# Kernel tuning notes

Measured on AMD Instinct MI355X. Metric: run time of the kernel, lower is better.

The kernel has to match this reference:

```python
import jax, jax.numpy as jnp
import numpy as np

DIST_SCALE = 10000.0   # divisor in kernel()
KERNEL_EPS = 0.0001    # additive epsilon before reciprocal


def setup_inputs() -> dict:
    key = jax.random.key(0)
    k1, k2, k3 = jax.random.split(key, 3)
    batch, keysize, dict_size, categories = 4096, 512, 16384, 128
    x = jax.random.normal(k1, (batch, keysize), dtype=jnp.float32)
    # keras TruncatedNormal(mean=0, stddev=3) approximated by scaled normal
    keys = 3.0 * jax.random.normal(k2, (dict_size, keysize), dtype=jnp.float32)
    V = jax.random.normal(k3, (dict_size, categories), dtype=jnp.float32)
    return {"x": x, "keys": keys, "V": V}


def reference(x, keys, V):
    # sq_distance(keys, x): (dict_size, batch)
    sq = (
        jnp.sum(keys * keys, axis=1, keepdims=True)            # (D, 1)
        - 2.0 * jnp.einsum("dk,bk->db", keys, x)               # (D, B)
        + jnp.sum(x * x, axis=1)[None, :]                      # (1, B)
    )
    kern = 1.0 / (sq / DIST_SCALE + KERNEL_EPS)                # (D, B)
    KV = jnp.einsum("db,dc->bc", kern, V)                      # (B, C)
    # original: diag(1 / (KV @ ones)) @ KV  ==  row-normalize by row sum
    return KV / jnp.sum(KV, axis=1, keepdims=True)
```

## Files before the change

kernel.cpp:

```cpp
#include <hip/hip_runtime.h>

#define BATCH 4096
#define DICT  16384
#define KDIM  512
#define CAT   128
#define ND    16
#define DSLICE (DICT/ND)
#define DCH   64
#define BT    256

typedef __attribute__((ext_vector_type(4))) float          f32x4;
typedef __attribute__((ext_vector_type(8))) short          short8;
typedef __attribute__((ext_vector_type(8))) unsigned short ushort8;
typedef __attribute__((ext_vector_type(4))) int            intx4;

__device__ __forceinline__ unsigned short f2bf(float f) {
  unsigned int u = __float_as_uint(f);
  return (unsigned short)((u + 0x7fffu + ((u >> 16) & 1u)) >> 16);
}

__device__ __forceinline__ unsigned int cvtpk_bf16(float lo, float hi) {
  unsigned int r;
  asm volatile("v_cvt_pk_bf16_f32 %0, %1, %2" : "=v"(r) : "v"(lo), "v"(hi));
  return r;
}

#define AS1 __attribute__((address_space(1)))
#define AS3 __attribute__((address_space(3)))
__device__ __forceinline__ void gl_lds16(const void* g, void* l) {
  __builtin_amdgcn_global_load_lds((AS1 void*)(g), (AS3 void*)(l), 16, 0, 0);
}

template <int N>
__device__ __forceinline__ void waitv() {
  if constexpr (N == 0)      asm volatile("s_waitcnt vmcnt(0)" ::: "memory");
  else if constexpr (N == 5) asm volatile("s_waitcnt vmcnt(5)" ::: "memory");
  else                       asm volatile("s_waitcnt vmcnt(6)" ::: "memory");
  __builtin_amdgcn_sched_barrier(0);
}

#define MFMA16(a, b, c) __builtin_amdgcn_mfma_f32_16x16x32_bf16((a), (b), (c), 0, 0, 0)

__global__ void prep_rows(const float* __restrict__ in,
                          unsigned short* __restrict__ ob,
                          float* __restrict__ sums) {
  const int lane = threadIdx.x & 63, wv = threadIdx.x >> 6;
  const int row = blockIdx.x * 4 + wv;
  const float* rp = in + ((size_t)row << 9);
  float4 a = *(const float4*)(rp + lane * 8);
  float4 b = *(const float4*)(rp + lane * 8 + 4);
  float s = a.x*a.x + a.y*a.y + a.z*a.z + a.w*a.w
          + b.x*b.x + b.y*b.y + b.z*b.z + b.w*b.w;
  ushort8 o;
  o[0]=f2bf(a.x); o[1]=f2bf(a.y); o[2]=f2bf(a.z); o[3]=f2bf(a.w);
  o[4]=f2bf(b.x); o[5]=f2bf(b.y); o[6]=f2bf(b.z); o[7]=f2bf(b.w);
  *(ushort8*)(ob + ((size_t)row << 9) + lane * 8) = o;
  #pragma unroll
  for (int m = 32; m; m >>= 1) s += __shfl_xor(s, m);
  if (lane == 0) sums[row] = s;
}

__global__ void prep_vt(const float* __restrict__ V,
                        unsigned short* __restrict__ Vt) {
  __shared__ float t[64][129];
  const int d0 = blockIdx.x * 64;
  const int tid = threadIdx.x;
  #pragma unroll
  for (int j = 0; j < 32; ++j) {
    int idx = j * 256 + tid;
    t[idx >> 7][idx & 127] = V[((size_t)d0 << 7) + idx];
  }
  __syncthreads();
  #pragma unroll
  for (int j = 0; j < 32; ++j) {
    int idx = j * 256 + tid;
    int cc = idx >> 6, dd = idx & 63;
    int p = dd & 31, qq = p >> 3, jj = p & 7;
    int src = (dd & 32) + 4 * qq + ((jj < 4) ? jj : (12 + jj));
    Vt[((size_t)cc << 14) + d0 + dd] = f2bf(t[src][cc]);
  }
}

__global__ __launch_bounds__(512, 2)
void varkeys_fused(const unsigned short* __restrict__ xb,
                   const unsigned short* __restrict__ kb,
                   const unsigned short* __restrict__ vt,
                   const float* __restrict__ sx,
                   const float* __restrict__ sk,
                   float* __restrict__ kvp) {
  __shared__ __attribute__((aligned(16))) char lds[131072];
  char* const VsB = lds + 81920;

  const int tid  = threadIdx.x;
  const int lane = tid & 63;
  const int wv   = tid >> 6;
  const int c    = lane & 15;
  const int h    = lane >> 4;
  const int sw   = (lane & 7) << 4;
  const int l3   = lane >> 3;

  const int bid    = blockIdx.x;
  const int btile  = bid & 15;
  const int dslice = bid >> 4;
  const int b0     = btile * BT;
  const int dbase  = dslice * DSLICE;

  const float sxv0 = sx[b0 + wv * 32 + c];
  const float sxv1 = sx[b0 + wv * 32 + 16 + c];

  const int rowA  = wv * 8 + l3;
  const int rowB0 = wv * 32 + l3;
  const int ofs   = (((lane & 7) ^ l3) << 4);

  const char* xbB = (const char*)xb;
  const char* kbB = (const char*)kb;
  const char* vtB = (const char*)vt;

  const f32x4 zero = {0.f, 0.f, 0.f, 0.f};
  f32x4 acc[2][8];
  #pragma unroll
  for (int i = 0; i < 2; ++i)
    #pragma unroll
    for (int j = 0; j < 8; ++j) acc[i][j] = zero;

  gl_lds16(kbB + ((size_t)(dbase + rowA) << 10) + ofs, lds + wv * 1024);
  #pragma unroll
  for (int r = 0; r < 4; ++r)
    gl_lds16(xbB + ((size_t)(b0 + rowB0 + r * 8) << 10) + ofs,
             lds + 16384 + (wv * 4 + r) * 1024);

  f32x4 skq[4];

  for (int dc = 0; dc < DSLICE / DCH; ++dc) {
    const int dg = dbase + dc * DCH;

    f32x4 S[4][2];
    #pragma unroll
    for (int i = 0; i < 4; ++i) { S[i][0] = zero; S[i][1] = zero; }

    #pragma unroll
    for (int kk = 0; kk < 8; ++kk) {
      __builtin_amdgcn_s_barrier();
      if (kk == 0) {
        #pragma unroll
        for (int i = 0; i < 4; ++i)
          skq[i] = *(const f32x4*)(sk + dg + i * 16 + h * 4);
      }
      if (!(kk == 7 && dc == (DSLICE / DCH - 1))) {
        const int dg2 = (kk == 7) ? dg + DCH : dg;
        const int kb2 = ((kk + 1) & 7) << 7;
        char* A2 = lds + ((kk + 1) & 1) * 8192;
        char* B2 = lds + 16384 + ((kk + 1) & 1) * 32768;
        gl_lds16(kbB + ((size_t)(dg2 + rowA) << 10) + kb2 + ofs, A2 + wv * 1024);
        #pragma unroll
        for (int r = 0; r < 4; ++r)
          gl_lds16(xbB + ((size_t)(b0 + rowB0 + r * 8) << 10) + kb2 + ofs,
                   B2 + (wv * 4 + r) * 1024);
        if (kk == 3)
          gl_lds16(vtB + ((size_t)(wv * 8 + l3) << 15) + ((size_t)dg << 1) + ofs,
                   VsB + wv * 1024);
        if (kk == 4)
          gl_lds16(vtB + ((size_t)(64 + wv * 8 + l3) << 15) + ((size_t)dg << 1) + ofs,
                   VsB + 8192 + wv * 1024);
      }
      if (kk == 7) { if (dc == DSLICE / DCH - 1) waitv<0>(); else waitv<5>(); }
      else if (kk == 3 || kk == 4) waitv<6>();
      else waitv<5>();
      __builtin_amdgcn_s_barrier();
      __builtin_amdgcn_sched_barrier(0);

      const char* As = lds + (kk & 1) * 8192;
      const char* Bs = lds + 16384 + (kk & 1) * 32768;
      #pragma unroll
      for (int kf = 0; kf < 2; ++kf) {
        const int ko = (kf * 64 + h * 16) ^ sw;
        short8 bf0 = *(const short8*)(Bs + ((wv * 32 + c) << 7) + ko);
        short8 bf1 = *(const short8*)(Bs + ((wv * 32 + 16 + c) << 7) + ko);
        #pragma unroll
        for (int i = 0; i < 4; ++i) {
          short8 af = *(const short8*)(As + ((i * 16 + c) << 7) + ko);
          S[i][0] = MFMA16(af, bf0, S[i][0]);
          S[i][1] = MFMA16(af, bf1, S[i][1]);
        }
      }
    }

    #pragma unroll
    for (int dk = 0; dk < 2; ++dk) {
      short8 pa[2];
      #pragma unroll
      for (int fj = 0; fj < 2; ++fj) {
        const float sxv = fj ? sxv1 : sxv0;
        const f32x4 sA = S[2 * dk][fj];
        const f32x4 sB = S[2 * dk + 1][fj];
        const f32x4 kA = skq[2 * dk];
        const f32x4 kB = skq[2 * dk + 1];
        float a0 = 10000.f * __builtin_amdgcn_rcpf(kA[0] + sxv - 2.f * sA[0] + 1.f);
        float a1 = 10000.f * __builtin_amdgcn_rcpf(kA[1] + sxv - 2.f * sA[1] + 1.f);
        float a2 = 10000.f * __builtin_amdgcn_rcpf(kA[2] + sxv - 2.f * sA[2] + 1.f);
        float a3 = 10000.f * __builtin_amdgcn_rcpf(kA[3] + sxv - 2.f * sA[3] + 1.f);
        float b0f = 10000.f * __builtin_amdgcn_rcpf(kB[0] + sxv - 2.f * sB[0] + 1.f);
        float b1f = 10000.f * __builtin_amdgcn_rcpf(kB[1] + sxv - 2.f * sB[1] + 1.f);
        float b2f = 10000.f * __builtin_amdgcn_rcpf(kB[2] + sxv - 2.f * sB[2] + 1.f);
        float b3f = 10000.f * __builtin_amdgcn_rcpf(kB[3] + sxv - 2.f * sB[3] + 1.f);
        intx4 fw;
        fw[0] = (int)cvtpk_bf16(a0, a1);
        fw[1] = (int)cvtpk_bf16(a2, a3);
        fw[2] = (int)cvtpk_bf16(b0f, b1f);
        fw[3] = (int)cvtpk_bf16(b2f, b3f);
        pa[fj] = *(short8*)&fw;
      }
      const int ko = (dk * 64 + h * 16) ^ sw;
      #pragma unroll
      for (int fc = 0; fc < 8; ++fc) {
        short8 vb = *(const short8*)(VsB + ((fc * 16 + c) << 7) + ko);
        acc[0][fc] = MFMA16(pa[0], vb, acc[0][fc]);
        acc[1][fc] = MFMA16(pa[1], vb, acc[1][fc]);
      }
    }
  }

  __syncthreads();
  float* eb = (float*)(lds + (wv << 14));
  #pragma unroll
  for (int fb = 0; fb < 2; ++fb)
    #pragma unroll
    for (int r = 0; r < 4; ++r) {
      const int brow = fb * 16 + h * 4 + r;
      #pragma unroll
      for (int fc = 0; fc < 8; ++fc)
        eb[(brow << 7) + fc * 16 + c] = acc[fb][fc][r];
    }
  float* op = kvp + (((size_t)dslice * BATCH + b0 + wv * 32) << 7);
  #pragma unroll
  for (int t = 0; t < 16; ++t) {
    const int row = t * 2 + (lane >> 5);
    f32x4 v = *(const f32x4*)(eb + (row << 7) + ((lane & 31) << 2));
    *(f32x4*)(op + (((size_t)row) << 7) + ((lane & 31) << 2)) = v;
  }
}

__global__ void reduce_norm(const float* __restrict__ part, float* __restrict__ out) {
  const int lane = threadIdx.x & 63, wv = threadIdx.x >> 6;
  const int b = blockIdx.x * 4 + wv;
  float v0 = 0.f, v1 = 0.f;
  #pragma unroll
  for (int s = 0; s < ND; ++s) {
    const float* p = part + ((((size_t)s << 12) + b) << 7);
    v0 += p[lane]; v1 += p[lane + 64];
  }
  float t = v0 + v1;
  #pragma unroll
  for (int m = 32; m; m >>= 1) t += __shfl_xor(t, m);
  out[((size_t)b << 7) + lane]      = v0 / t;
  out[((size_t)b << 7) + lane + 64] = v1 / t;
}

extern "C" void kernel_launch(void* const* d_in, const int* in_sizes, int n_in,
                              void* d_out, int out_size, void* d_ws, size_t ws_size,
                              hipStream_t stream) {
  (void)in_sizes; (void)n_in; (void)out_size; (void)ws_size;
  const float* x    = (const float*)d_in[0];
  const float* keys = (const float*)d_in[1];
  const float* V    = (const float*)d_in[2];
  float* out = (float*)d_out;
  char* ws = (char*)d_ws;
  unsigned short* xb = (unsigned short*)(ws);
  unsigned short* kb = (unsigned short*)(ws + ((size_t)4 << 20));
  unsigned short* vt = (unsigned short*)(ws + ((size_t)20 << 20));
  float* sx  = (float*)(ws + ((size_t)24 << 20));
  float* sk  = (float*)(ws + ((size_t)24 << 20) + (1 << 16));
  float* kvp = (float*)(ws + ((size_t)25 << 20));

  prep_rows<<<BATCH / 4, 256, 0, stream>>>(x, xb, sx);
  prep_rows<<<DICT / 4, 256, 0, stream>>>(keys, kb, sk);
  prep_vt<<<DICT / 64, 256, 0, stream>>>(V, vt);
  varkeys_fused<<<(BATCH / BT) * ND, 512, 0, stream>>>(xb, kb, vt, sx, sk, kvp);
  reduce_norm<<<BATCH / 4, 256, 0, stream>>>(kvp, out);
}
```

Before: 135.1 us.

## Enlarge per-wave tile to 128x64 with 4 waves per block

Each workgroup now uses 256 threads (4 waves) and processes a 128-wide dictionary chunk. Each wave computes a 128x64 distance tile instead of 64x32, and the V tile is split into two halves loaded across k-steps. The goal is more MFMA work per LDS fragment load and fewer barriers per unit of compute, which raises register-level reuse. In exchange, accumulators and S tiles grow to about 256 AGPR/VGPR values per lane, which risks spills and low occupancy (one block per CU). The epilogue now stores the output through LDS cooperatively across the whole block.

After: 157.7 us. 16.7% more time.

```diff
diff --git a/kernel.cpp b/kernel.cpp
--- a/kernel.cpp
+++ b/kernel.cpp
@@ -6,7 +6,7 @@
 #define CAT   128
 #define ND    16
 #define DSLICE (DICT/ND)
-#define DCH   64
+#define DCH   128
 #define BT    256
 
 typedef __attribute__((ext_vector_type(4))) float          f32x4;
@@ -33,9 +33,9 @@
 
 template <int N>
 __device__ __forceinline__ void waitv() {
-  if constexpr (N == 0)      asm volatile("s_waitcnt vmcnt(0)" ::: "memory");
-  else if constexpr (N == 5) asm volatile("s_waitcnt vmcnt(5)" ::: "memory");
-  else                       asm volatile("s_waitcnt vmcnt(6)" ::: "memory");
+  if constexpr (N == 0)       asm volatile("s_waitcnt vmcnt(0)" ::: "memory");
+  else if constexpr (N == 12) asm volatile("s_waitcnt vmcnt(12)" ::: "memory");
+  else                        asm volatile("s_waitcnt vmcnt(14)" ::: "memory");
   __builtin_amdgcn_sched_barrier(0);
 }
 
@@ -81,7 +81,7 @@
   }
 }
 
-__global__ __launch_bounds__(512, 2)
+__global__ __launch_bounds__(256, 1)
 void varkeys_fused(const unsigned short* __restrict__ xb,
                    const unsigned short* __restrict__ kb,
                    const unsigned short* __restrict__ vt,
@@ -89,7 +89,8 @@
                    const float* __restrict__ sk,
                    float* __restrict__ kvp) {
   __shared__ __attribute__((aligned(16))) char lds[131072];
-  char* const VsB = lds + 81920;
+  char* const VsA = lds + 98304;
+  char* const VsB = lds + 114688;
 
   const int tid  = threadIdx.x;
   const int lane = tid & 63;
@@ -105,138 +106,158 @@
   const int b0     = btile * BT;
   const int dbase  = dslice * DSLICE;
 
-  const float sxv0 = sx[b0 + wv * 32 + c];
-  const float sxv1 = sx[b0 + wv * 32 + 16 + c];
-
-  const int rowA  = wv * 8 + l3;
-  const int rowB0 = wv * 32 + l3;
-  const int ofs   = (((lane & 7) ^ l3) << 4);
+  float sxv[4];
+  #pragma unroll
+  for (int fj = 0; fj < 4; ++fj) sxv[fj] = sx[b0 + wv * 64 + fj * 16 + c];
+
+  const int rowS = wv * 8 + l3;
+  const int ofs  = (((lane & 7) ^ l3) << 4);
 
   const char* xbB = (const char*)xb;
   const char* kbB = (const char*)kb;
   const char* vtB = (const char*)vt;
 
   const f32x4 zero = {0.f, 0.f, 0.f, 0.f};
-  f32x4 acc[2][8];
-  #pragma unroll
-  for (int i = 0; i < 2; ++i)
-    #pragma unroll
-    for (int j = 0; j < 8; ++j) acc[i][j] = zero;
-
-  gl_lds16(kbB + ((size_t)(dbase + rowA) << 10) + ofs, lds + wv * 1024);
-  #pragma unroll
-  for (int r = 0; r < 4; ++r)
-    gl_lds16(xbB + ((size_t)(b0 + rowB0 + r * 8) << 10) + ofs,
-             lds + 16384 + (wv * 4 + r) * 1024);
-
-  f32x4 skq[4];
+  f32x4 acc[4][8];
+  #pragma unroll
+  for (int j = 0; j < 4; ++j)
+    #pragma unroll
+    for (int n = 0; n < 8; ++n) acc[j][n] = zero;
+
+  auto stageAB = [&](int ns) {
+    const int dg2 = dbase + (ns >> 3) * DCH;
+    const int kb2 = (ns & 7) << 7;
+    char* A2 = lds + (ns & 1) * 16384;
+    char* B2 = lds + 32768 + (ns & 1) * 32768;
+    #pragma unroll
+    for (int cl = 0; cl < 4; ++cl)
+      gl_lds16(kbB + ((size_t)(dg2 + cl * 32 + rowS) << 10) + kb2 + ofs,
+               A2 + cl * 4096 + wv * 1024);
+    #pragma unroll
+    for (int cl = 0; cl < 8; ++cl)
+      gl_lds16(xbB + ((size_t)(b0 + cl * 32 + rowS) << 10) + kb2 + ofs,
+               B2 + cl * 4096 + wv * 1024);
+  };
+
+  stageAB(0);
+
+  f32x4 skq[8];
 
   for (int dc = 0; dc < DSLICE / DCH; ++dc) {
     const int dg = dbase + dc * DCH;
 
-    f32x4 S[4][2];
-    #pragma unroll
-    for (int i = 0; i < 4; ++i) { S[i][0] = zero; S[i][1] = zero; }
+    f32x4 S[8][4];
+    #pragma unroll
+    for (int i = 0; i < 8; ++i)
+      #pragma unroll
+      for (int fj = 0; fj < 4; ++fj) S[i][fj] = zero;
 
     #pragma unroll
     for (int kk = 0; kk < 8; ++kk) {
       __builtin_amdgcn_s_barrier();
       if (kk == 0) {
         #pragma unroll
-        for (int i = 0; i < 4; ++i)
+        for (int i = 0; i < 8; ++i)
           skq[i] = *(const f32x4*)(sk + dg + i * 16 + h * 4);
       }
-      if (!(kk == 7 && dc == (DSLICE / DCH - 1))) {
-        const int dg2 = (kk == 7) ? dg + DCH : dg;
-        const int kb2 = ((kk + 1) & 7) << 7;
-        char* A2 = lds + ((kk + 1) & 1) * 8192;
-        char* B2 = lds + 16384 + ((kk + 1) & 1) * 32768;
-        gl_lds16(kbB + ((size_t)(dg2 + rowA) << 10) + kb2 + ofs, A2 + wv * 1024);
-        #pragma unroll
-        for (int r = 0; r < 4; ++r)
-          gl_lds16(xbB + ((size_t)(b0 + rowB0 + r * 8) << 10) + kb2 + ofs,
-                   B2 + (wv * 4 + r) * 1024);
-        if (kk == 3)
-          gl_lds16(vtB + ((size_t)(wv * 8 + l3) << 15) + ((size_t)dg << 1) + ofs,
-                   VsB + wv * 1024);
-        if (kk == 4)
-          gl_lds16(vtB + ((size_t)(64 + wv * 8 + l3) << 15) + ((size_t)dg << 1) + ofs,
-                   VsB + 8192 + wv * 1024);
+      const int ns = dc * 8 + kk + 1;
+      if (ns < 64) stageAB(ns);
+      if (kk >= 2 && kk <= 5) {
+        char* const VsH = (kk < 4) ? VsA : VsB;
+        const int hv = (kk < 4) ? 0 : 1;
+        #pragma unroll
+        for (int t = 0; t < 2; ++t) {
+          const int cl = ((kk - 2) & 1) * 2 + t;
+          gl_lds16(vtB + ((size_t)(cl * 32 + rowS) << 15)
+                       + ((size_t)(dg + hv * 64) << 1) + ofs,
+                   VsH + cl * 4096 + wv * 1024);
+        }
       }
-      if (kk == 7) { if (dc == DSLICE / DCH - 1) waitv<0>(); else waitv<5>(); }
-      else if (kk == 3 || kk == 4) waitv<6>();
-      else waitv<5>();
+      if (ns == 64) waitv<0>();
+      else if (kk >= 2 && kk <= 5) waitv<14>();
+      else waitv<12>();
       __builtin_amdgcn_s_barrier();
       __builtin_amdgcn_sched_barrier(0);
 
-      const char* As = lds + (kk & 1) * 8192;
-      const char* Bs = lds + 16384 + (kk & 1) * 32768;
+      const char* As = lds + (kk & 1) * 16384;
+      const char* Bs = lds + 32768 + (kk & 1) * 32768;
       #pragma unroll
       for (int kf = 0; kf < 2; ++kf) {
         const int ko = (kf * 64 + h * 16) ^ sw;
-        short8 bf0 = *(const short8*)(Bs + ((wv * 32 + c) << 7) + ko);
-        short8 bf1 = *(const short8*)(Bs + ((wv * 32 + 16 + c) << 7) + ko);
-        #pragma unroll
-        for (int i = 0; i < 4; ++i) {
+        short8 bf[4];
+        #pragma unroll
+        for (int fj = 0; fj < 4; ++fj)
+          bf[fj] = *(const short8*)(Bs + ((wv * 64 + fj * 16 + c) << 7) + ko);
+        #pragma unroll
+        for (int i = 0; i < 8; ++i) {
           short8 af = *(const short8*)(As + ((i * 16 + c) << 7) + ko);
-          S[i][0] = MFMA16(af, bf0, S[i][0]);
-          S[i][1] = MFMA16(af, bf1, S[i][1]);
+          #pragma unroll
+          for (int fj = 0; fj < 4; ++fj)
+            S[i][fj] = MFMA16(af, bf[fj], S[i][fj]);
         }
       }
     }
 
     #pragma unroll
-    for (int dk = 0; dk < 2; ++dk) {
-      short8 pa[2];
+    for (int hv = 0; hv < 2; ++hv) {
+      const char* VsH = hv ? VsB : VsA;
       #pragma unroll
-      for (int fj = 0; fj < 2; ++fj) {
-        const float sxv = fj ? sxv1 : sxv0;
-        const f32x4 sA = S[2 * dk][fj];
-        const f32x4 sB = S[2 * dk + 1][fj];
-        const f32x4 kA = skq[2 * dk];
-        const f32x4 kB = skq[2 * dk + 1];
-        float a0 = 10000.f * __builtin_amdgcn_rcpf(kA[0] + sxv - 2.f * sA[0] + 1.f);
-        float a1 = 10000.f * __builtin_amdgcn_rcpf(kA[1] + sxv - 2.f * sA[1] + 1.f);
-        float a2 = 10000.f * __builtin_amdgcn_rcpf(kA[2] + sxv - 2.f * sA[2] + 1.f);
-        float a3 = 10000.f * __builtin_amdgcn_rcpf(kA[3] + sxv - 2.f * sA[3] + 1.f);
-        float b0f = 10000.f * __builtin_amdgcn_rcpf(kB[0] + sxv - 2.f * sB[0] + 1.f);
-        float b1f = 10000.f * __builtin_amdgcn_rcpf(kB[1] + sxv - 2.f * sB[1] + 1.f);
-        float b2f = 10000.f * __builtin_amdgcn_rcpf(kB[2] + sxv - 2.f * sB[2] + 1.f);
-        float b3f = 10000.f * __builtin_amdgcn_rcpf(kB[3] + sxv - 2.f * sB[3] + 1.f);
-        intx4 fw;
-        fw[0] = (int)cvtpk_bf16(a0, a1);
-        fw[1] = (int)cvtpk_bf16(a2, a3);
-        fw[2] = (int)cvtpk_bf16(b0f, b1f);
-        fw[3] = (int)cvtpk_bf16(b2f, b3f);
-        pa[fj] = *(short8*)&fw;
-      }
-      const int ko = (dk * 64 + h * 16) ^ sw;
-      #pragma unroll
-      for (int fc = 0; fc < 8; ++fc) {
-        short8 vb = *(const short8*)(VsB + ((fc * 16 + c) << 7) + ko);
-        acc[0][fc] = MFMA16(pa[0], vb, acc[0][fc]);
-        acc[1][fc] = MFMA16(pa[1], vb, acc[1][fc]);
+      for (int dkh = 0; dkh < 2; ++dkh) {
+        const int dk = hv * 2 + dkh;
+        short8 pa[4];
+        #pragma unroll
+        for (int fj = 0; fj < 4; ++fj) {
+          const float sv = sxv[fj];
+          const f32x4 sA = S[2 * dk][fj];
+          const f32x4 sB = S[2 * dk + 1][fj];
+          const f32x4 kA = skq[2 * dk];
+          const f32x4 kB = skq[2 * dk + 1];
+          float a0 = 10000.f * __builtin_amdgcn_rcpf(kA[0] + sv - 2.f * sA[0] + 1.f);
+          float a1 = 10000.f * __builtin_amdgcn_rcpf(kA[1] + sv - 2.f * sA[1] + 1.f);
+          float a2 = 10000.f * __builtin_amdgcn_rcpf(kA[2] + sv - 2.f * sA[2] + 1.f);
+          float a3 = 10000.f * __builtin_amdgcn_rcpf(kA[3] + sv - 2.f * sA[3] + 1.f);
+          float b0f = 10000.f * __builtin_amdgcn_rcpf(kB[0] + sv - 2.f * sB[0] + 1.f);
+          float b1f = 10000.f * __builtin_amdgcn_rcpf(kB[1] + sv - 2.f * sB[1] + 1.f);
+          float b2f = 10000.f * __builtin_amdgcn_rcpf(kB[2] + sv - 2.f * sB[2] + 1.f);
+          float b3f = 10000.f * __builtin_amdgcn_rcpf(kB[3] + sv - 2.f * sB[3] + 1.f);
+          intx4 fw;
+          fw[0] = (int)cvtpk_bf16(a0, a1);
+          fw[1] = (int)cvtpk_bf16(a2, a3);
+          fw[2] = (int)cvtpk_bf16(b0f, b1f);
+          fw[3] = (int)cvtpk_bf16(b2f, b3f);
+          pa[fj] = *(short8*)&fw;
+        }
+        const int ko = (dkh * 64 + h * 16) ^ sw;
+        #pragma unroll
+        for (int fc = 0; fc < 8; ++fc) {
+          short8 vb = *(const short8*)(VsH + ((fc * 16 + c) << 7) + ko);
+          #pragma unroll
+          for (int fj = 0; fj < 4; ++fj)
+            acc[fj][fc] = MFMA16(pa[fj], vb, acc[fj][fc]);
+        }
       }
     }
   }
 
   __syncthreads();
-  float* eb = (float*)(lds + (wv << 14));
-  #pragma unroll
-  for (int fb = 0; fb < 2; ++fb)
+  float* eb = (float*)(lds + (wv << 15));
+  #pragma unroll
+  for (int fj = 0; fj < 4; ++fj)
     #pragma unroll
     for (int r = 0; r < 4; ++r) {
-      const int brow = fb * 16 + h * 4 + r;
+      const int brow = fj * 16 + h * 4 + r;
       #pragma unroll
       for (int fc = 0; fc < 8; ++fc)
-        eb[(brow << 7) + fc * 16 + c] = acc[fb][fc][r];
+        eb[(brow << 7) + fc * 16 + c] = acc[fj][fc][r];
     }
-  float* op = kvp + (((size_t)dslice * BATCH + b0 + wv * 32) << 7);
-  #pragma unroll
-  for (int t = 0; t < 16; ++t) {
-    const int row = t * 2 + (lane >> 5);
-    f32x4 v = *(const f32x4*)(eb + (row << 7) + ((lane & 31) << 2));
-    *(f32x4*)(op + (((size_t)row) << 7) + ((lane & 31) << 2)) = v;
+  __syncthreads();
+  float* op = kvp + (((size_t)dslice * BATCH + b0) << 7);
+  const float* ebase = (const float*)lds;
+  #pragma unroll
+  for (int t = 0; t < 32; ++t) {
+    const int row = t * 8 + (tid >> 5);
+    f32x4 v = *(const f32x4*)(ebase + (row << 7) + ((tid & 31) << 2));
+    *(f32x4*)(op + (((size_t)row) << 7) + ((tid & 31) << 2)) = v;
   }
 }
 
@@ -275,6 +296,6 @@
   prep_rows<<<BATCH / 4, 256, 0, stream>>>(x, xb, sx);
   prep_rows<<<DICT / 4, 256, 0, stream>>>(keys, kb, sk);
   prep_vt<<<DICT / 64, 256, 0, stream>>>(V, vt);
-  varkeys_fused<<<(BATCH / BT) * ND, 512, 0, stream>>>(xb, kb, vt, sx, sk, kvp);
+  varkeys_fused<<<(BATCH / BT) * ND, 256, 0, stream>>>(xb, kb, vt, sx, sk, kvp);
   reduce_norm<<<BATCH / 4, 256, 0, stream>>>(kvp, out);
 }
```
